# Kernel optimization log

Hardware: AMD Instinct MI355X
Metric: run time of the kernel (lower is better)

## Reference

```python
import jax, jax.numpy as jnp
import numpy as np

N_NODES = 100000
N_EDGES = 1600000
N_GRAPHS = 5000
NODE_DIM = 16
EDGE_DIM = 16
HID = 20


def setup_inputs() -> dict:
    key = jax.random.key(0)
    ks = jax.random.split(key, 12)
    edge_index = jax.random.randint(ks[0], (2, N_EDGES), 0, N_NODES)
    node_attr = jax.random.normal(ks[1], (N_NODES, NODE_DIM), dtype=jnp.float32)
    edge_attr = jax.random.normal(ks[2], (N_EDGES, EDGE_DIM), dtype=jnp.float32)
    batch = jnp.sort(jax.random.randint(ks[3], (N_NODES,), 0, N_GRAPHS))
    s = 0.1
    W_msg = jax.random.normal(ks[4], (2 * NODE_DIM + EDGE_DIM, HID), dtype=jnp.float32) * s
    b_msg = jnp.zeros((HID,), dtype=jnp.float32)
    W1 = jax.random.normal(ks[5], (HID, 10), dtype=jnp.float32) * s
    b1 = jnp.zeros((10,), dtype=jnp.float32)
    W2 = jax.random.normal(ks[6], (10, 10), dtype=jnp.float32) * s
    b2 = jnp.zeros((10,), dtype=jnp.float32)
    W3 = jax.random.normal(ks[7], (10, 1), dtype=jnp.float32) * s
    b3 = jnp.zeros((1,), dtype=jnp.float32)
    return {"edge_index": edge_index, "node_attr": node_attr, "edge_attr": edge_attr,
            "batch": batch, "W_msg": W_msg, "b_msg": b_msg, "W1": W1, "b1": b1,
            "W2": W2, "b2": b2, "W3": W3, "b3": b3}


def reference(edge_index, node_attr, edge_attr, batch,
              W_msg, b_msg, W1, b1, W2, b2, W3, b3):
    src, dst = edge_index[0], edge_index[1]
    # MPL_1: gather -> linear -> relu -> scatter-sum to destination nodes
    feats = jnp.concatenate([node_attr[src], node_attr[dst], edge_attr], axis=-1)  # [E, 48]
    msg = jax.nn.relu(feats @ W_msg + b_msg)  # [E, 20]
    x = jax.ops.segment_sum(msg, dst, num_segments=N_NODES)  # [N, 20]
    # node MLP + graph pooling (segment_coo sum over batch) + graph MLP
    x = jax.nn.relu(x @ W1 + b1)  # [N, 10]
    g = jax.ops.segment_sum(x, batch, num_segments=N_GRAPHS)  # [G, 10]
    g = jax.nn.relu(g @ W2 + b2)
    return g @ W3 + b3  # [G, 1]
```

## Files before the change

### kernel.cpp

```cpp
#include <hip/hip_runtime.h>

constexpr int NN = 100000;
constexpr int NE = 1600000;
constexpr int NG = 5000;
constexpr int BKT = 64;
constexpr int NBKT = (NN + BKT - 1) / BKT;
constexpr int NB = 128;
constexpr int CHUNK = NE / NB;

typedef float v2f __attribute__((ext_vector_type(2)));

constexpr size_t OFF_G  = 0;
constexpr size_t OFF_BH = 50048;
constexpr size_t OFF_ST = OFF_BH + (size_t)NB * NBKT;
constexpr size_t OFF_PM = OFF_ST + NBKT + 1;

__global__ __launch_bounds__(256) void k_hist(const int* __restrict__ ei,
                                              int* __restrict__ bh,
                                              float* __restrict__ g) {
  __shared__ int lh[NBKT];
  for (int i = threadIdx.x; i < NBKT; i += 256) lh[i] = 0;
  __syncthreads();
  const int* dstp = ei + NE;
  int s = blockIdx.x * CHUNK;
  for (int i = s + threadIdx.x; i < s + CHUNK; i += 256)
    atomicAdd(&lh[dstp[i] >> 6], 1);
  int gid = blockIdx.x * 256 + threadIdx.x;
  if (gid < 12500) ((float4*)g)[gid] = make_float4(0.f, 0.f, 0.f, 0.f);
  __syncthreads();
  int* out = bh + (size_t)blockIdx.x * NBKT;
  for (int k = threadIdx.x; k < NBKT; k += 256) out[k] = lh[k];
}

__global__ __launch_bounds__(256) void k_btot(const int* __restrict__ bh,
                                              int* __restrict__ starts) {
  int k = blockIdx.x * 256 + threadIdx.x;
  if (k >= NBKT) return;
  int tot = 0;
  for (int b = 0; b < NB; b += 4) {
    int a0 = bh[(size_t)(b    ) * NBKT + k];
    int a1 = bh[(size_t)(b + 1) * NBKT + k];
    int a2 = bh[(size_t)(b + 2) * NBKT + k];
    int a3 = bh[(size_t)(b + 3) * NBKT + k];
    tot += a0 + a1 + a2 + a3;
  }
  starts[k] = tot;
}

__global__ __launch_bounds__(1024) void k_sscan(int* __restrict__ starts) {
  __shared__ int s0[1024], s1[1024];
  int t = threadIdx.x;
  int k0 = 2 * t, k1 = 2 * t + 1;
  int tot0 = (k0 < NBKT) ? starts[k0] : 0;
  int tot1 = (k1 < NBKT) ? starts[k1] : 0;
  int ssum = tot0 + tot1;
  int* cur = s0; int* nxt = s1;
  cur[t] = ssum;
  __syncthreads();
  for (int off = 1; off < 1024; off <<= 1) {
    int v = cur[t];
    if (t >= off) v += cur[t - off];
    nxt[t] = v;
    __syncthreads();
    int* tmp = cur; cur = nxt; nxt = tmp;
  }
  int excl = cur[t] - ssum;
  if (k0 < NBKT) starts[k0] = excl;
  if (k1 <= NBKT) starts[k1] = excl + tot0;
}

__global__ __launch_bounds__(256) void k_bases(int* __restrict__ bh,
                                               const int* __restrict__ starts) {
  int k = blockIdx.x * 256 + threadIdx.x;
  if (k >= NBKT) return;
  int run = starts[k];
  for (int b = 0; b < NB; ++b) {
    size_t idx = (size_t)b * NBKT + k;
    int v = bh[idx];
    bh[idx] = run;
    run += v;
  }
}

__global__ __launch_bounds__(256) void k_scatter(const int* __restrict__ ei,
                                                 const int* __restrict__ bh,
                                                 int* __restrict__ perm) {
  __shared__ int base[NBKT];
  __shared__ int cnt[NBKT];
  const int* row = bh + (size_t)blockIdx.x * NBKT;
  for (int k = threadIdx.x; k < NBKT; k += 256) { base[k] = row[k]; cnt[k] = 0; }
  __syncthreads();
  const int* dstp = ei + NE;
  int s = blockIdx.x * CHUNK;
  for (int i = s + threadIdx.x; i < s + CHUNK; i += 256) {
    int d = dstp[i];
    int k = d >> 6;
    int r = atomicAdd(&cnt[k], 1);
    perm[base[k] + r] = i | ((d & 63) << 24);
  }
}

#define PK4(V, K0) \
  a0 = __builtin_elementwise_fma(v2f{(V).x, (V).x}, W[K0+0], a0); \
  a1 = __builtin_elementwise_fma(v2f{(V).y, (V).y}, W[K0+1], a1); \
  a2 = __builtin_elementwise_fma(v2f{(V).z, (V).z}, W[K0+2], a2); \
  a3 = __builtin_elementwise_fma(v2f{(V).w, (V).w}, W[K0+3], a3);

__global__ __launch_bounds__(512, 1) void k_edge(
    const int* __restrict__ ei,
    const float* __restrict__ nattr,
    const float* __restrict__ eattr,
    const float* __restrict__ Wm,
    const float* __restrict__ bm,
    const int* __restrict__ batch,
    const float* __restrict__ W1,
    const float* __restrict__ b1,
    const int* __restrict__ perm,
    const int* __restrict__ starts,
    float* __restrict__ g) {
  __shared__ float xt[20 * 65];
  __shared__ float gb[64 * 10];
  __shared__ float4 wt4[250];
  __shared__ float4 us4[64 * 5];
  __shared__ float4 feat[8 * 54];
  __shared__ int s_se[2];
  __shared__ int s_bmin;
  int tid = threadIdx.x;
  for (int i = tid; i < 20 * 65; i += 512) xt[i] = 0.f;
  for (int i = tid; i < 640; i += 512) gb[i] = 0.f;
  if (tid < 240) {
    int j = tid / 24, t = tid - j * 24, k = 2 * t;
    wt4[j * 25 + t] = make_float4(Wm[k * 20 + 2 * j],       Wm[k * 20 + 2 * j + 1],
                                  Wm[(k + 1) * 20 + 2 * j], Wm[(k + 1) * 20 + 2 * j + 1]);
  }
  int nbase = blockIdx.x * BKT;
  if (tid < 256) {
    int dl = tid >> 2, part = tid & 3;
    int row = min(nbase + dl, NN - 1);
    us4[dl * 5 + part] = ((const float4*)nattr)[(size_t)row * 4 + part];
  }
  if (tid < 2) s_se[tid] = starts[blockIdx.x + tid];
  if (tid == 0) s_bmin = batch[nbase];
  __syncthreads();
  int is = s_se[0], ie = s_se[1];

  int wave = tid >> 6;
  int lane = tid & 63;
  int ep = lane / 10;
  int jp = lane - ep * 10;
  bool act = ep < 6;
  int epc = act ? ep : 0;

  v2f bj = {bm[2 * jp], bm[2 * jp + 1]};

  v2f W[48];
#pragma unroll
  for (int t = 0; t < 24; ++t) {
    float4 q = wt4[jp * 25 + t];
    W[2 * t]     = v2f{q.x, q.y};
    W[2 * t + 1] = v2f{q.z, q.w};
  }
#pragma unroll
  for (int k = 0; k < 48; ++k) asm volatile("" : "+v"(W[k]));

  int ce = lane >> 3, cpart = lane & 7;
  bool ldr = lane < 48;
  int esrc = (ldr ? ce : 0) * 10;
  int fbase = wave * 54;

  int base = is + wave * 6;
  int p0 = 0, p1 = 0, p2 = 0, svn = 0;
  float4 st = make_float4(0.f, 0.f, 0.f, 0.f);
  if (base < ie) {
    p0 = perm[min(base + epc, ie - 1)];
    p1 = (base + 48 < ie) ? perm[min(base + 48 + epc, ie - 1)] : p0;
    p2 = (base + 96 < ie) ? perm[min(base + 96 + epc, ie - 1)] : p1;
    int sv0 = ei[p0 & 0xFFFFFF];
    svn     = ei[p1 & 0xFFFFFF];
    int pp = __shfl(p0, esrc);
    int ss = __shfl(sv0, esrc);
    if (ldr) {
      const float4* a = (cpart < 4)
          ? ((const float4*)eattr) + (size_t)(pp & 0xFFFFFF) * 4 + cpart
          : ((const float4*)nattr) + (size_t)ss * 4 + (cpart - 4);
      st = *a;
    }
  }
  while (base < ie) {
    if (ldr) feat[fbase + ce * 9 + cpart] = st;
    int pp = __shfl(p1, esrc);
    int ss = __shfl(svn, esrc);
    int p3 = (base + 144 < ie) ? perm[min(base + 144 + epc, ie - 1)] : p2;
    int svn2 = ei[p2 & 0xFFFFFF];
    if (ldr) {
      const float4* a = (cpart < 4)
          ? ((const float4*)eattr) + (size_t)(pp & 0xFFFFFF) * 4 + cpart
          : ((const float4*)nattr) + (size_t)ss * 4 + (cpart - 4);
      st = *a;
    }
    int dl = (p0 >> 24) & 63;
    int frow = fbase + ep * 9;
    float4 e0 = feat[frow + 0], e1 = feat[frow + 1], e2 = feat[frow + 2], e3 = feat[frow + 3];
    float4 n0 = feat[frow + 4], n1 = feat[frow + 5], n2 = feat[frow + 6], n3 = feat[frow + 7];
    float4 u0 = us4[dl * 5 + 0], u1 = us4[dl * 5 + 1], u2 = us4[dl * 5 + 2], u3 = us4[dl * 5 + 3];

    v2f a0 = {0.f, 0.f}, a1 = {0.f, 0.f}, a2 = {0.f, 0.f}, a3 = {0.f, 0.f};
    PK4(n0, 0)  PK4(n1, 4)  PK4(n2, 8)  PK4(n3, 12)
    PK4(u0, 16) PK4(u1, 20) PK4(u2, 24) PK4(u3, 28)
    PK4(e0, 32) PK4(e1, 36) PK4(e2, 40) PK4(e3, 44)
    v2f r = ((a0 + a1) + (a2 + a3)) + bj;

    bool valid = act && (base + epc < ie);
    float m0 = fmaxf(r.x, 0.f);
    float m1 = fmaxf(r.y, 0.f);
    if (valid && m0 > 0.f) atomicAdd(&xt[(2 * jp) * 65 + dl], m0);
    if (valid && m1 > 0.f) atomicAdd(&xt[(2 * jp + 1) * 65 + dl], m1);

    base += 48; p0 = p1; p1 = p2; p2 = p3; svn = svn2;
  }
  __syncthreads();

  int nn = min(BKT, NN - nbase);
  int bmin = s_bmin;
  if (tid < 64 && tid < nn) {
    int node = tid;
    float xi[20];
#pragma unroll
    for (int j = 0; j < 20; ++j) xi[j] = xt[j * 65 + node];
    float acc[10];
#pragma unroll
    for (int j = 0; j < 10; ++j) acc[j] = b1[j];
#pragma unroll
    for (int k = 0; k < 20; ++k) {
      float fk = xi[k];
#pragma unroll
      for (int j = 0; j < 10; ++j) acc[j] = fmaf(fk, W1[k * 10 + j], acc[j]);
    }
    int bn = batch[nbase + node];
    int d = bn - bmin;
    if (d < 64) {
#pragma unroll
      for (int j = 0; j < 10; ++j) {
        float m = fmaxf(acc[j], 0.f);
        if (m > 0.f) atomicAdd(&gb[d * 10 + j], m);
      }
    } else {
#pragma unroll
      for (int j = 0; j < 10; ++j) {
        float m = fmaxf(acc[j], 0.f);
        if (m > 0.f) unsafeAtomicAdd(&g[(size_t)bn * 10 + j], m);
      }
    }
  }
  __syncthreads();
  int glim = min(640, NG * 10 - bmin * 10);
  float* gp = g + (size_t)bmin * 10;
  for (int idx = tid; idx < glim; idx += 512) {
    float v = gb[idx];
    if (v != 0.f) unsafeAtomicAdd(&gp[idx], v);
  }
}

__global__ __launch_bounds__(256) void k_graph(
    const float* __restrict__ g,
    const float* __restrict__ W2, const float* __restrict__ b2,
    const float* __restrict__ W3, const float* __restrict__ b3,
    float* __restrict__ out) {
  int i = blockIdx.x * 256 + threadIdx.x;
  if (i >= NG) return;
  float gi[10];
  const float2* pg = (const float2*)(g + (size_t)i * 10);
#pragma unroll
  for (int k = 0; k < 5; ++k) { float2 v = pg[k]; gi[2*k] = v.x; gi[2*k+1] = v.y; }
  float o = b3[0];
#pragma unroll
  for (int j = 0; j < 10; ++j) {
    float a = b2[j];
#pragma unroll
    for (int k = 0; k < 10; ++k) a = fmaf(gi[k], W2[k * 10 + j], a);
    o = fmaf(fmaxf(a, 0.f), W3[j], o);
  }
  out[i] = o;
}

extern "C" void kernel_launch(void* const* d_in, const int* in_sizes, int n_in,
                              void* d_out, int out_size, void* d_ws, size_t ws_size,
                              hipStream_t stream) {
  const int*   ei    = (const int*)  d_in[0];
  const float* nattr = (const float*)d_in[1];
  const float* eattr = (const float*)d_in[2];
  const int*   batch = (const int*)  d_in[3];
  const float* Wm    = (const float*)d_in[4];
  const float* bm    = (const float*)d_in[5];
  const float* W1    = (const float*)d_in[6];
  const float* b1    = (const float*)d_in[7];
  const float* W2    = (const float*)d_in[8];
  const float* b2    = (const float*)d_in[9];
  const float* W3    = (const float*)d_in[10];
  const float* b3    = (const float*)d_in[11];

  float* g      = (float*)d_ws + OFF_G;
  int*   bh     = (int*)d_ws + OFF_BH;
  int*   starts = (int*)d_ws + OFF_ST;
  int*   perm   = (int*)d_ws + OFF_PM;

  constexpr int SCAN_BLKS = (NBKT + 255) / 256;

  k_hist   <<<NB, 256, 0, stream>>>(ei, bh, g);
  k_btot   <<<SCAN_BLKS, 256, 0, stream>>>(bh, starts);
  k_sscan  <<<1, 1024, 0, stream>>>(starts);
  k_bases  <<<SCAN_BLKS, 256, 0, stream>>>(bh, starts);
  k_scatter<<<NB, 256, 0, stream>>>(ei, bh, perm);
  k_edge   <<<NBKT, 512, 0, stream>>>(ei, nattr, eattr, Wm, bm, batch, W1, b1,
                                      perm, starts, g);
  k_graph  <<<(NG + 255) / 256, 256, 0, stream>>>(g, W2, b2, W3, b3, (float*)d_out);
}
```

Before: 392.5 us.

## Pre-sort edge attributes into destination-bucket order before the edge kernel

Adds an inverse-permutation scatter and a new reorder kernel that copies edge attributes and source indices into bucket-sorted order. The edge kernel can then read edge features contiguously and drop one level of dependent indirection (perm→ei→nattr). The cost is an extra full pass over the ~100MB of edge attributes, with a random-scatter write, plus a large workspace requirement. The path is chosen at runtime from the workspace size, falling back to the old path.

```diff
diff --git a/kernel.cpp b/kernel.cpp
--- a/kernel.cpp
+++ b/kernel.cpp
@@ -14,6 +14,9 @@
 constexpr size_t OFF_BH = 50048;
 constexpr size_t OFF_ST = OFF_BH + (size_t)NB * NBKT;
 constexpr size_t OFF_PM = OFF_ST + NBKT + 1;
+constexpr size_t OFF_SP = OFF_PM + NE;
+constexpr size_t OFF_EP = ((OFF_SP + NE) + 15) & ~(size_t)15;
+constexpr size_t NEED_WORDS = OFF_EP + (size_t)NE * 16;
 
 __global__ __launch_bounds__(256) void k_hist(const int* __restrict__ ei,
                                               int* __restrict__ bh,
@@ -82,9 +85,10 @@
   }
 }
 
+template <bool PRE>
 __global__ __launch_bounds__(256) void k_scatter(const int* __restrict__ ei,
                                                  const int* __restrict__ bh,
-                                                 int* __restrict__ perm) {
+                                                 int* __restrict__ pm) {
   __shared__ int base[NBKT];
   __shared__ int cnt[NBKT];
   const int* row = bh + (size_t)blockIdx.x * NBKT;
@@ -96,8 +100,25 @@
     int d = dstp[i];
     int k = d >> 6;
     int r = atomicAdd(&cnt[k], 1);
-    perm[base[k] + r] = i | ((d & 63) << 24);
-  }
+    int slot = base[k] + r;
+    if (PRE) pm[i] = slot | ((d & 63) << 25);
+    else     pm[slot] = i | ((d & 63) << 24);
+  }
+}
+
+__global__ __launch_bounds__(256) void k_reorder(const int* __restrict__ ei,
+                                                 const float* __restrict__ eattr,
+                                                 const int* __restrict__ inv,
+                                                 float* __restrict__ ep_,
+                                                 int* __restrict__ srcp) {
+  int gid = blockIdx.x * 256 + threadIdx.x;
+  int e = gid >> 2, part = gid & 3;
+  if (e >= NE) return;
+  int iv = inv[e];
+  int slot = iv & 0x1FFFFFF;
+  float4 v = ((const float4*)eattr)[(size_t)e * 4 + part];
+  ((float4*)ep_)[(size_t)slot * 4 + part] = v;
+  if (part == 0) srcp[slot] = ei[e] | ((iv >> 25) << 24);
 }
 
 #define PK4(V, K0) \
@@ -106,6 +127,7 @@
   a2 = __builtin_elementwise_fma(v2f{(V).z, (V).z}, W[K0+2], a2); \
   a3 = __builtin_elementwise_fma(v2f{(V).w, (V).w}, W[K0+3], a3);
 
+template <bool PRE>
 __global__ __launch_bounds__(512, 1) void k_edge(
     const int* __restrict__ ei,
     const float* __restrict__ nattr,
@@ -115,7 +137,7 @@
     const int* __restrict__ batch,
     const float* __restrict__ W1,
     const float* __restrict__ b1,
-    const int* __restrict__ perm,
+    const int* __restrict__ pm,
     const int* __restrict__ starts,
     float* __restrict__ g) {
   __shared__ float xt[20 * 65];
@@ -169,54 +191,96 @@
   int fbase = wave * 54;
 
   int base = is + wave * 6;
-  int p0 = 0, p1 = 0, p2 = 0, svn = 0;
-  float4 st = make_float4(0.f, 0.f, 0.f, 0.f);
-  if (base < ie) {
-    p0 = perm[min(base + epc, ie - 1)];
-    p1 = (base + 48 < ie) ? perm[min(base + 48 + epc, ie - 1)] : p0;
-    p2 = (base + 96 < ie) ? perm[min(base + 96 + epc, ie - 1)] : p1;
-    int sv0 = ei[p0 & 0xFFFFFF];
-    svn     = ei[p1 & 0xFFFFFF];
-    int pp = __shfl(p0, esrc);
-    int ss = __shfl(sv0, esrc);
-    if (ldr) {
-      const float4* a = (cpart < 4)
-          ? ((const float4*)eattr) + (size_t)(pp & 0xFFFFFF) * 4 + cpart
-          : ((const float4*)nattr) + (size_t)ss * 4 + (cpart - 4);
-      st = *a;
-    }
-  }
-  while (base < ie) {
-    if (ldr) feat[fbase + ce * 9 + cpart] = st;
-    int pp = __shfl(p1, esrc);
-    int ss = __shfl(svn, esrc);
-    int p3 = (base + 144 < ie) ? perm[min(base + 144 + epc, ie - 1)] : p2;
-    int svn2 = ei[p2 & 0xFFFFFF];
-    if (ldr) {
-      const float4* a = (cpart < 4)
-          ? ((const float4*)eattr) + (size_t)(pp & 0xFFFFFF) * 4 + cpart
-          : ((const float4*)nattr) + (size_t)ss * 4 + (cpart - 4);
-      st = *a;
-    }
-    int dl = (p0 >> 24) & 63;
-    int frow = fbase + ep * 9;
-    float4 e0 = feat[frow + 0], e1 = feat[frow + 1], e2 = feat[frow + 2], e3 = feat[frow + 3];
-    float4 n0 = feat[frow + 4], n1 = feat[frow + 5], n2 = feat[frow + 6], n3 = feat[frow + 7];
-    float4 u0 = us4[dl * 5 + 0], u1 = us4[dl * 5 + 1], u2 = us4[dl * 5 + 2], u3 = us4[dl * 5 + 3];
-
-    v2f a0 = {0.f, 0.f}, a1 = {0.f, 0.f}, a2 = {0.f, 0.f}, a3 = {0.f, 0.f};
-    PK4(n0, 0)  PK4(n1, 4)  PK4(n2, 8)  PK4(n3, 12)
-    PK4(u0, 16) PK4(u1, 20) PK4(u2, 24) PK4(u3, 28)
-    PK4(e0, 32) PK4(e1, 36) PK4(e2, 40) PK4(e3, 44)
-    v2f r = ((a0 + a1) + (a2 + a3)) + bj;
-
-    bool valid = act && (base + epc < ie);
-    float m0 = fmaxf(r.x, 0.f);
-    float m1 = fmaxf(r.y, 0.f);
-    if (valid && m0 > 0.f) atomicAdd(&xt[(2 * jp) * 65 + dl], m0);
-    if (valid && m1 > 0.f) atomicAdd(&xt[(2 * jp + 1) * 65 + dl], m1);
-
-    base += 48; p0 = p1; p1 = p2; p2 = p3; svn = svn2;
+  if (PRE) {
+    int sp0 = 0, sp1 = 0;
+    float4 st = make_float4(0.f, 0.f, 0.f, 0.f);
+    if (base < ie) {
+      sp0 = pm[min(base + epc, ie - 1)];
+      sp1 = (base + 48 < ie) ? pm[min(base + 48 + epc, ie - 1)] : sp0;
+      int ss = __shfl(sp0, esrc) & 0xFFFFFF;
+      if (ldr) {
+        st = (cpart < 4)
+          ? ((const float4*)eattr)[(size_t)min(base + ce, ie - 1) * 4 + cpart]
+          : ((const float4*)nattr)[(size_t)ss * 4 + (cpart - 4)];
+      }
+    }
+    while (base < ie) {
+      if (ldr) feat[fbase + ce * 9 + cpart] = st;
+      int ss = __shfl(sp1, esrc) & 0xFFFFFF;
+      int sp2 = (base + 96 < ie) ? pm[min(base + 96 + epc, ie - 1)] : sp1;
+      if (ldr) {
+        st = (cpart < 4)
+          ? ((const float4*)eattr)[(size_t)min(base + 48 + ce, ie - 1) * 4 + cpart]
+          : ((const float4*)nattr)[(size_t)ss * 4 + (cpart - 4)];
+      }
+      int dl = (sp0 >> 24) & 63;
+      int frow = fbase + ep * 9;
+      float4 e0 = feat[frow + 0], e1 = feat[frow + 1], e2 = feat[frow + 2], e3 = feat[frow + 3];
+      float4 n0 = feat[frow + 4], n1 = feat[frow + 5], n2 = feat[frow + 6], n3 = feat[frow + 7];
+      float4 u0 = us4[dl * 5 + 0], u1 = us4[dl * 5 + 1], u2 = us4[dl * 5 + 2], u3 = us4[dl * 5 + 3];
+
+      v2f a0 = {0.f, 0.f}, a1 = {0.f, 0.f}, a2 = {0.f, 0.f}, a3 = {0.f, 0.f};
+      PK4(n0, 0)  PK4(n1, 4)  PK4(n2, 8)  PK4(n3, 12)
+      PK4(u0, 16) PK4(u1, 20) PK4(u2, 24) PK4(u3, 28)
+      PK4(e0, 32) PK4(e1, 36) PK4(e2, 40) PK4(e3, 44)
+      v2f r = ((a0 + a1) + (a2 + a3)) + bj;
+
+      bool valid = act && (base + epc < ie);
+      float m0 = fmaxf(r.x, 0.f);
+      float m1 = fmaxf(r.y, 0.f);
+      if (valid && m0 > 0.f) atomicAdd(&xt[(2 * jp) * 65 + dl], m0);
+      if (valid && m1 > 0.f) atomicAdd(&xt[(2 * jp + 1) * 65 + dl], m1);
+
+      base += 48; sp0 = sp1; sp1 = sp2;
+    }
+  } else {
+    int p0 = 0, p1 = 0, p2 = 0, svn = 0;
+    float4 st = make_float4(0.f, 0.f, 0.f, 0.f);
+    if (base < ie) {
+      p0 = pm[min(base + epc, ie - 1)];
+      p1 = (base + 48 < ie) ? pm[min(base + 48 + epc, ie - 1)] : p0;
+      p2 = (base + 96 < ie) ? pm[min(base + 96 + epc, ie - 1)] : p1;
+      int sv0 = ei[p0 & 0xFFFFFF];
+      svn     = ei[p1 & 0xFFFFFF];
+      int pp = __shfl(p0, esrc);
+      int ss = __shfl(sv0, esrc);
+      if (ldr) {
+        st = (cpart < 4)
+          ? ((const float4*)eattr)[(size_t)(pp & 0xFFFFFF) * 4 + cpart]
+          : ((const float4*)nattr)[(size_t)ss * 4 + (cpart - 4)];
+      }
+    }
+    while (base < ie) {
+      if (ldr) feat[fbase + ce * 9 + cpart] = st;
+      int pp = __shfl(p1, esrc);
+      int ss = __shfl(svn, esrc);
+      int p3 = (base + 144 < ie) ? pm[min(base + 144 + epc, ie - 1)] : p2;
+      int svn2 = ei[p2 & 0xFFFFFF];
+      if (ldr) {
+        st = (cpart < 4)
+          ? ((const float4*)eattr)[(size_t)(pp & 0xFFFFFF) * 4 + cpart]
+          : ((const float4*)nattr)[(size_t)ss * 4 + (cpart - 4)];
+      }
+      int dl = (p0 >> 24) & 63;
+      int frow = fbase + ep * 9;
+      float4 e0 = feat[frow + 0], e1 = feat[frow + 1], e2 = feat[frow + 2], e3 = feat[frow + 3];
+      float4 n0 = feat[frow + 4], n1 = feat[frow + 5], n2 = feat[frow + 6], n3 = feat[frow + 7];
+      float4 u0 = us4[dl * 5 + 0], u1 = us4[dl * 5 + 1], u2 = us4[dl * 5 + 2], u3 = us4[dl * 5 + 3];
+
+      v2f a0 = {0.f, 0.f}, a1 = {0.f, 0.f}, a2 = {0.f, 0.f}, a3 = {0.f, 0.f};
+      PK4(n0, 0)  PK4(n1, 4)  PK4(n2, 8)  PK4(n3, 12)
+      PK4(u0, 16) PK4(u1, 20) PK4(u2, 24) PK4(u3, 28)
+      PK4(e0, 32) PK4(e1, 36) PK4(e2, 40) PK4(e3, 44)
+      v2f r = ((a0 + a1) + (a2 + a3)) + bj;
+
+      bool valid = act && (base + epc < ie);
+      float m0 = fmaxf(r.x, 0.f);
+      float m1 = fmaxf(r.y, 0.f);
+      if (valid && m0 > 0.f) atomicAdd(&xt[(2 * jp) * 65 + dl], m0);
+      if (valid && m1 > 0.f) atomicAdd(&xt[(2 * jp + 1) * 65 + dl], m1);
+
+      base += 48; p0 = p1; p1 = p2; p2 = p3; svn = svn2;
+    }
   }
   __syncthreads();
 
@@ -302,7 +366,11 @@
   float* g      = (float*)d_ws + OFF_G;
   int*   bh     = (int*)d_ws + OFF_BH;
   int*   starts = (int*)d_ws + OFF_ST;
-  int*   perm   = (int*)d_ws + OFF_PM;
+  int*   pm     = (int*)d_ws + OFF_PM;
+  int*   srcp   = (int*)d_ws + OFF_SP;
+  float* ep_    = (float*)d_ws + OFF_EP;
+
+  bool pre = ws_size >= NEED_WORDS * 4;
 
   constexpr int SCAN_BLKS = (NBKT + 255) / 256;
 
@@ -310,8 +378,15 @@
   k_btot   <<<SCAN_BLKS, 256, 0, stream>>>(bh, starts);
   k_sscan  <<<1, 1024, 0, stream>>>(starts);
   k_bases  <<<SCAN_BLKS, 256, 0, stream>>>(bh, starts);
-  k_scatter<<<NB, 256, 0, stream>>>(ei, bh, perm);
-  k_edge   <<<NBKT, 512, 0, stream>>>(ei, nattr, eattr, Wm, bm, batch, W1, b1,
-                                      perm, starts, g);
+  if (pre) {
+    k_scatter<true><<<NB, 256, 0, stream>>>(ei, bh, pm);
+    k_reorder<<<(NE * 4 + 255) / 256, 256, 0, stream>>>(ei, eattr, pm, ep_, srcp);
+    k_edge<true><<<NBKT, 512, 0, stream>>>(ei, nattr, ep_, Wm, bm, batch, W1, b1,
+                                           srcp, starts, g);
+  } else {
+    k_scatter<false><<<NB, 256, 0, stream>>>(ei, bh, pm);
+    k_edge<false><<<NBKT, 512, 0, stream>>>(ei, nattr, eattr, Wm, bm, batch, W1, b1,
+                                            pm, starts, g);
+  }
   k_graph  <<<(NG + 255) / 256, 256, 0, stream>>>(g, W2, b2, W3, b3, (float*)d_out);
 }
```

Result: slower. 440.2 us (+12.1%).
